# Kernel tuning notes

Measured on AMD Instinct MI355X. Metric: run time of the kernel, lower is better.

The kernel has to match this reference:

```python
import jax, jax.numpy as jnp
import numpy as np

N_NODES = 50000
N_EDGES = 640000
IN_FEATS = 128
HID = 128


def setup_inputs() -> dict:
    key = jax.random.key(0)
    ks = jax.random.split(key, 8)
    x = jax.random.normal(ks[0], (N_NODES, IN_FEATS), dtype=jnp.float32)
    src = jax.random.randint(ks[1], (N_EDGES,), 0, N_NODES, dtype=jnp.int32)
    dst = jax.random.randint(ks[2], (N_EDGES,), 0, N_NODES, dtype=jnp.int32)
    s1 = 1.0 / np.sqrt(IN_FEATS)
    s2 = 1.0 / np.sqrt(HID)
    W1 = jax.random.normal(ks[3], (IN_FEATS, HID), dtype=jnp.float32) * s1
    b1 = jnp.zeros((HID,), dtype=jnp.float32)
    W2 = jax.random.normal(ks[4], (HID, HID), dtype=jnp.float32) * s2
    b2 = jnp.zeros((HID,), dtype=jnp.float32)
    Wr = jax.random.normal(ks[5], (HID, 2), dtype=jnp.float32) * s2
    br = jnp.zeros((2,), dtype=jnp.float32)
    return {"x": x, "src": src, "dst": dst, "W1": W1, "b1": b1,
            "W2": W2, "b2": b2, "Wr": Wr, "br": br}


def _degree_norm(idx, n):
    # D^{-1/2}, with 0 for zero-degree nodes (DGL sets inf -> 0)
    deg = jax.ops.segment_sum(jnp.ones(idx.shape[0], jnp.float32), idx, num_segments=n)
    return jnp.where(deg > 0, jax.lax.rsqrt(jnp.maximum(deg, 1.0)), 0.0)


def _graph_conv(h, W, b, src, dst, norm_out, norm_in, n):
    # DGL GraphConv, norm='both': out = D_in^{-1/2} A D_out^{-1/2} (h W) + b
    hW = (h * norm_out[:, None]) @ W          # [N, hid]
    agg = jax.ops.segment_sum(hW[src], dst, num_segments=n)  # gather+scatter over edges
    return agg * norm_in[:, None] + b


def reference(x, src, dst, W1, b1, W2, b2, Wr, br):
    n = x.shape[0]
    norm_out = _degree_norm(src, n)  # source-side out-degree norm
    norm_in = _degree_norm(dst, n)   # dest-side in-degree norm
    h = jax.nn.relu(_graph_conv(x, W1, b1, src, dst, norm_out, norm_in, n))
    h = jax.nn.relu(_graph_conv(h, W2, b2, src, dst, norm_out, norm_in, n))
    hg = jnp.mean(h, axis=0, keepdims=True)  # [1, hid]
    return hg @ Wr + br                      # [1, 2]
```

## Files before the change

kernel.cpp:

```cpp
#include <hip/hip_runtime.h>
#include <hip/hip_bf16.h>

#define FEAT 128
#define RBITS 13
#define RSIZE 8192
#define NCHUNK 64

typedef __attribute__((ext_vector_type(8))) short short8;
typedef __attribute__((ext_vector_type(4))) short short4v;
typedef __attribute__((ext_vector_type(4))) float f32x4;

__device__ __forceinline__ ushort f2bf(float f) {
    union { float f; unsigned u; } v; v.f = f;
    unsigned u = v.u;
    unsigned r = 0x7fffu + ((u >> 16) & 1u);
    return (ushort)((u + r) >> 16);
}
__device__ __forceinline__ float bf2f(short s) {
    union { unsigned u; float f; } v;
    v.u = ((unsigned)(ushort)s) << 16;
    return v.f;
}

__global__ __launch_bounds__(256)
void hist_kernel(const int* __restrict__ src, const int* __restrict__ dst,
                 unsigned* __restrict__ partialSrc, unsigned* __restrict__ partialDst,
                 int E, int CS)
{
    __shared__ unsigned hs[RSIZE / 4];
    __shared__ unsigned hd[RSIZE / 4];
    const int c = blockIdx.x, p = blockIdx.y;
    for (int r = threadIdx.x; r < RSIZE / 4; r += 256) { hs[r] = 0; hd[r] = 0; }
    __syncthreads();
    const int e0 = c * CS, e1 = min(E, e0 + CS);
    for (int e = e0 + threadIdx.x; e < e1; e += 256) {
        int s = src[e];
        if ((s >> RBITS) == p) {
            int r = s & (RSIZE - 1);
            atomicAdd(&hs[r >> 2], 1u << ((r & 3) * 8));
        }
        int d = dst[e];
        if ((d >> RBITS) == p) {
            int r = d & (RSIZE - 1);
            atomicAdd(&hd[r >> 2], 1u << ((r & 3) * 8));
        }
    }
    __syncthreads();
    const size_t base = ((size_t)p * NCHUNK + c) * (RSIZE / 4);
    for (int r = threadIdx.x; r < RSIZE / 4; r += 256) {
        partialSrc[base + r] = hs[r];
        partialDst[base + r] = hd[r];
    }
}

__global__ __launch_bounds__(256)
void merge_kernel(const unsigned char* __restrict__ ps8, unsigned char* __restrict__ pd8,
                  int* __restrict__ cntIn, float* __restrict__ normOut,
                  float* __restrict__ normIn, int* __restrict__ blockSums, int N)
{
    const int n = blockIdx.x * 256 + threadIdx.x;
    unsigned off = 0;
    if (n < N) {
        const int p = n >> RBITS, r = n & (RSIZE - 1);
        const size_t base = (size_t)p * NCHUNK * RSIZE + r;
        unsigned so = 0;
#pragma unroll 8
        for (int c = 0; c < NCHUNK; ++c) so += ps8[base + (size_t)c * RSIZE];
#pragma unroll 8
        for (int c = 0; c < NCHUNK; ++c) {
            size_t i = base + (size_t)c * RSIZE;
            unsigned t = pd8[i];
            pd8[i] = (unsigned char)off;
            off += t;
        }
        cntIn[n]   = (int)off;
        normIn[n]  = off ? rsqrtf((float)off) : 0.0f;
        normOut[n] = so  ? rsqrtf((float)so)  : 0.0f;
    }
    __shared__ int sh[256];
    sh[threadIdx.x] = (int)off;
    __syncthreads();
    for (int o = 128; o > 0; o >>= 1) {
        if (threadIdx.x < o) sh[threadIdx.x] += sh[threadIdx.x + o];
        __syncthreads();
    }
    if (threadIdx.x == 0) blockSums[blockIdx.x] = sh[0];
}

__global__ __launch_bounds__(256)
void rowstart_kernel(const int* __restrict__ cntIn, const int* __restrict__ blockSums,
                     int* __restrict__ rowStart, float* __restrict__ colsum,
                     int N, int NB, int E)
{
    __shared__ int bs[256];
    __shared__ int bse[256];
    __shared__ int sh[256];
    const int t = threadIdx.x;
    int bv = (t < NB) ? blockSums[t] : 0;
    bs[t] = bv;
    __syncthreads();
    for (int off = 1; off < 256; off <<= 1) {
        int u = (t >= off) ? bs[t - off] : 0;
        __syncthreads();
        bs[t] += u;
        __syncthreads();
    }
    bse[t] = bs[t] - bv;
    __syncthreads();

    const int i = blockIdx.x * 256 + t;
    int v = (i < N) ? cntIn[i] : 0;
    sh[t] = v;
    __syncthreads();
    for (int off = 1; off < 256; off <<= 1) {
        int u = (t >= off) ? sh[t - off] : 0;
        __syncthreads();
        sh[t] += u;
        __syncthreads();
    }
    if (i < N) rowStart[i] = bse[blockIdx.x] + sh[t] - v;
    if (blockIdx.x == 0) {
        if (t == 0) rowStart[N] = E;
        colsum[t] = 0.0f;
    }
}

__global__ __launch_bounds__(256)
void fill_kernel(const int* __restrict__ src, const int* __restrict__ dst,
                 const int* __restrict__ rowStart, const unsigned char* __restrict__ chunkOff8,
                 int* __restrict__ csrSrc, int N, int E, int CS)
{
    __shared__ unsigned cursor[RSIZE];
    const int c = blockIdx.x, p = blockIdx.y;
    const unsigned char* co = chunkOff8 + ((size_t)p * NCHUNK + c) * RSIZE;
    for (int r = threadIdx.x; r < RSIZE; r += 256) {
        int n = (p << RBITS) + r;
        cursor[r] = (n < N) ? (unsigned)rowStart[n] + (unsigned)co[r] : 0u;
    }
    __syncthreads();
    const int e0 = c * CS, e1 = min(E, e0 + CS);
    for (int e = e0 + threadIdx.x; e < e1; e += 256) {
        int d = dst[e];
        if ((d >> RBITS) == p) {
            unsigned pos = atomicAdd(&cursor[d & (RSIZE - 1)], 1u);
            csrSrc[pos] = src[e];
        }
    }
}

template<bool F32IN>
__global__ __launch_bounds__(256)
void gemm_mfma_kernel(const void* __restrict__ Ain, const float* __restrict__ W,
                      const float* __restrict__ scale, ushort* __restrict__ C, int M)
{
    __shared__ ushort WT[128 * 132];
    __shared__ ushort As[64 * 132];
    __shared__ float  sScale[64];

    const int tid  = threadIdx.x;
    const int wv   = tid >> 6;
    const int lane = tid & 63;
    const int rowHalf = wv >> 1;
    const int colHalf = wv & 1;
    const int l15  = lane & 15;
    const int quad = lane >> 4;
    const int row0 = blockIdx.x << 6;

    for (int it = 0; it < 16; ++it) {
        int fid = tid + (it << 8);
        int k   = fid >> 5;
        int c4  = (fid & 31) << 2;
        float4 w = *(const float4*)(W + (size_t)k * FEAT + c4);
        WT[(c4 + 0) * 132 + k] = f2bf(w.x);
        WT[(c4 + 1) * 132 + k] = f2bf(w.y);
        WT[(c4 + 2) * 132 + k] = f2bf(w.z);
        WT[(c4 + 3) * 132 + k] = f2bf(w.w);
    }
#pragma unroll
    for (int it = 0; it < 4; ++it) {
        int fid = tid + (it << 8);
        int r   = fid >> 4;
        int seg = (fid & 15) << 3;
        int grow = row0 + r;
        short4v lo = {0, 0, 0, 0}, hi = {0, 0, 0, 0};
        if (grow < M) {
            if (F32IN) {
                const float* pa = (const float*)Ain + (size_t)grow * FEAT + seg;
                float4 u0 = *(const float4*)(pa);
                float4 u1 = *(const float4*)(pa + 4);
                lo[0] = (short)f2bf(u0.x); lo[1] = (short)f2bf(u0.y);
                lo[2] = (short)f2bf(u0.z); lo[3] = (short)f2bf(u0.w);
                hi[0] = (short)f2bf(u1.x); hi[1] = (short)f2bf(u1.y);
                hi[2] = (short)f2bf(u1.z); hi[3] = (short)f2bf(u1.w);
            } else {
                const ushort* pa = (const ushort*)Ain + (size_t)grow * FEAT + seg;
                lo = *(const short4v*)(pa);
                hi = *(const short4v*)(pa + 4);
            }
        }
        *(short4v*)&As[r * 132 + seg]     = lo;
        *(short4v*)&As[r * 132 + seg + 4] = hi;
    }
    if (tid < 64) {
        int grow = row0 + tid;
        sScale[tid] = (grow < M) ? scale[grow] : 0.0f;
    }
    __syncthreads();

    f32x4 acc[2][4] = {};
#pragma unroll
    for (int kst = 0; kst < 4; ++kst) {
        int k = kst * 32 + quad * 8;
        short8 af[2];
#pragma unroll
        for (int rt = 0; rt < 2; ++rt) {
            int row = rowHalf * 32 + rt * 16 + l15;
            short4v lo = *(const short4v*)&As[row * 132 + k];
            short4v hi = *(const short4v*)&As[row * 132 + k + 4];
            af[rt] = __builtin_shufflevector(lo, hi, 0, 1, 2, 3, 4, 5, 6, 7);
        }
        short8 bf[4];
#pragma unroll
        for (int ct = 0; ct < 4; ++ct) {
            int col = colHalf * 64 + ct * 16 + l15;
            short4v lo = *(const short4v*)&WT[col * 132 + k];
            short4v hi = *(const short4v*)&WT[col * 132 + k + 4];
            bf[ct] = __builtin_shufflevector(lo, hi, 0, 1, 2, 3, 4, 5, 6, 7);
        }
#pragma unroll
        for (int rt = 0; rt < 2; ++rt)
#pragma unroll
            for (int ct = 0; ct < 4; ++ct)
                acc[rt][ct] = __builtin_amdgcn_mfma_f32_16x16x32_bf16(
                    af[rt], bf[ct], acc[rt][ct], 0, 0, 0);
    }

#pragma unroll
    for (int rt = 0; rt < 2; ++rt) {
        int rbase = rowHalf * 32 + rt * 16 + quad * 4;
#pragma unroll
        for (int reg = 0; reg < 4; ++reg) {
            int rl = rbase + reg;
            int grow = row0 + rl;
            if (grow < M) {
                float sc = sScale[rl];
#pragma unroll
                for (int ct = 0; ct < 4; ++ct) {
                    int col = colHalf * 64 + ct * 16 + l15;
                    C[(size_t)grow * FEAT + col] = f2bf(acc[rt][ct][reg] * sc);
                }
            }
        }
    }
}

__global__ __launch_bounds__(256)
void gather_kernel(const ushort* __restrict__ t, const int* __restrict__ rowStart,
                   const int* __restrict__ csrSrc, const float* __restrict__ normIn,
                   const float* __restrict__ bias, ushort* __restrict__ out, int N)
{
    const int hw   = threadIdx.x >> 5;
    const int lane = threadIdx.x & 31;
    const int node = blockIdx.x * 8 + hw;
    if (node >= N) return;
    const int s = rowStart[node];
    const int e = rowStart[node + 1];
    float a0 = 0.f, a1 = 0.f, a2 = 0.f, a3 = 0.f;
    for (int base = s; base < e; base += 32) {
        const int m = min(32, e - base);
        int idx = (base + lane < e) ? csrSrc[base + lane] : 0;
        int j = 0;
        for (; j + 4 <= m; j += 4) {
            int s0 = __shfl(idx, j,     32);
            int s1 = __shfl(idx, j + 1, 32);
            int s2 = __shfl(idx, j + 2, 32);
            int s3 = __shfl(idx, j + 3, 32);
            short4v v0 = *(const short4v*)(t + (size_t)s0 * FEAT + lane * 4);
            short4v v1 = *(const short4v*)(t + (size_t)s1 * FEAT + lane * 4);
            short4v v2 = *(const short4v*)(t + (size_t)s2 * FEAT + lane * 4);
            short4v v3 = *(const short4v*)(t + (size_t)s3 * FEAT + lane * 4);
            a0 += bf2f(v0[0]) + bf2f(v1[0]) + bf2f(v2[0]) + bf2f(v3[0]);
            a1 += bf2f(v0[1]) + bf2f(v1[1]) + bf2f(v2[1]) + bf2f(v3[1]);
            a2 += bf2f(v0[2]) + bf2f(v1[2]) + bf2f(v2[2]) + bf2f(v3[2]);
            a3 += bf2f(v0[3]) + bf2f(v1[3]) + bf2f(v2[3]) + bf2f(v3[3]);
        }
        for (; j < m; ++j) {
            int srcn = __shfl(idx, j, 32);
            short4v v = *(const short4v*)(t + (size_t)srcn * FEAT + lane * 4);
            a0 += bf2f(v[0]); a1 += bf2f(v[1]); a2 += bf2f(v[2]); a3 += bf2f(v[3]);
        }
    }
    float ni = normIn[node];
    float4 b = *(const float4*)(bias + lane * 4);
    short4v o;
    o[0] = (short)f2bf(fmaxf(fmaf(a0, ni, b.x), 0.0f));
    o[1] = (short)f2bf(fmaxf(fmaf(a1, ni, b.y), 0.0f));
    o[2] = (short)f2bf(fmaxf(fmaf(a2, ni, b.z), 0.0f));
    o[3] = (short)f2bf(fmaxf(fmaf(a3, ni, b.w), 0.0f));
    *(short4v*)(out + (size_t)node * FEAT + lane * 4) = o;
}

__global__ __launch_bounds__(256)
void colreduce_kernel(const ushort* __restrict__ h2, float* __restrict__ colsum, int N)
{
    const int c  = threadIdx.x & 127;
    const int rg = threadIdx.x >> 7;
    const int r0 = blockIdx.x * 256;
    const int rEnd = min(r0 + 256, N);
    float acc = 0.0f;
    for (int r = r0 + rg; r < rEnd; r += 2)
        acc += bf2f(h2[(size_t)r * FEAT + c]);
    __shared__ float sh[256];
    sh[threadIdx.x] = acc;
    __syncthreads();
    if (rg == 0) unsafeAtomicAdd(&colsum[c], sh[c] + sh[128 + c]);
}

__global__ __launch_bounds__(128)
void final_kernel(const float* __restrict__ colsum, const float* __restrict__ Wr,
                  const float* __restrict__ br, float* __restrict__ out, float invN)
{
    __shared__ float s0[128], s1[128];
    int j = threadIdx.x;
    float hg = colsum[j] * invN;
    s0[j] = hg * Wr[2 * j + 0];
    s1[j] = hg * Wr[2 * j + 1];
    __syncthreads();
    for (int off = 64; off > 0; off >>= 1) {
        if (j < off) { s0[j] += s0[j + off]; s1[j] += s1[j + off]; }
        __syncthreads();
    }
    if (j == 0) {
        out[0] = s0[0] + br[0];
        out[1] = s1[0] + br[1];
    }
}

extern "C" void kernel_launch(void* const* d_in, const int* in_sizes, int n_in,
                              void* d_out, int out_size, void* d_ws, size_t ws_size,
                              hipStream_t stream)
{
    const float* x   = (const float*)d_in[0];
    const int*   src = (const int*)d_in[1];
    const int*   dst = (const int*)d_in[2];
    const float* W1  = (const float*)d_in[3];
    const float* b1  = (const float*)d_in[4];
    const float* W2  = (const float*)d_in[5];
    const float* b2  = (const float*)d_in[6];
    const float* Wr  = (const float*)d_in[7];
    const float* br  = (const float*)d_in[8];
    float* out = (float*)d_out;

    const int N = in_sizes[0] / FEAT;
    const int E = in_sizes[1];
    const int NP = ((N + 255) / 256) * 256;
    const int NB = (N + 255) / 256;
    const int P  = (N + RSIZE - 1) / RSIZE;
    const int CS = (E + NCHUNK - 1) / NCHUNK;

    char* p = (char*)d_ws;
    unsigned* partialSrc = (unsigned*)p;  p += (size_t)P * NCHUNK * (RSIZE / 4) * 4;
    unsigned* partialDst = (unsigned*)p;  p += (size_t)P * NCHUNK * (RSIZE / 4) * 4;
    float*  colsum    = (float*)p;        p += 256 * 4;
    int*    blockSums = (int*)p;          p += 256 * 4;
    int*    cntIn     = (int*)p;          p += (size_t)NP * 4;
    float*  normOut   = (float*)p;        p += (size_t)NP * 4;
    float*  normIn    = (float*)p;        p += (size_t)NP * 4;
    int*    rowStart  = (int*)p;          p += (size_t)(NP + 64) * 4;
    int*    csrSrc    = (int*)p;          p += (size_t)E * 4;
    ushort* bufT      = (ushort*)p;       p += (size_t)N * FEAT * 2;
    ushort* bufH      = (ushort*)p;       p += (size_t)N * FEAT * 2;

    hist_kernel<<<dim3(NCHUNK, P), 256, 0, stream>>>(src, dst, partialSrc, partialDst, E, CS);
    merge_kernel<<<NB, 256, 0, stream>>>((const unsigned char*)partialSrc,
                                         (unsigned char*)partialDst,
                                         cntIn, normOut, normIn, blockSums, N);
    rowstart_kernel<<<NB, 256, 0, stream>>>(cntIn, blockSums, rowStart, colsum, N, NB, E);
    fill_kernel<<<dim3(NCHUNK, P), 256, 0, stream>>>(src, dst, rowStart,
                                                     (const unsigned char*)partialDst,
                                                     csrSrc, N, E, CS);

    const int nStrips = (N + 63) / 64;
    const int gathBlocks = (N + 7) / 8;

    gemm_mfma_kernel<true><<<nStrips, 256, 0, stream>>>((const void*)x, W1, normOut, bufT, N);
    gather_kernel<<<gathBlocks, 256, 0, stream>>>(bufT, rowStart, csrSrc, normIn, b1, bufH, N);

    gemm_mfma_kernel<false><<<nStrips, 256, 0, stream>>>((const void*)bufH, W2, normOut, bufT, N);
    gather_kernel<<<gathBlocks, 256, 0, stream>>>(bufT, rowStart, csrSrc, normIn, b2, bufH, N);

    colreduce_kernel<<<NB, 256, 0, stream>>>(bufH, colsum, N);
    final_kernel<<<1, 128, 0, stream>>>(colsum, Wr, br, out, 1.0f / (float)N);
}
```

Before: 260.8 us.

## Restructure CSR build with whole-range byte histograms and pretransposed bf16 weights

The histogram and fill kernels drop the per-range partitioning (P ranges of 8192 nodes) and cover all nodes in one shared-memory array of packed byte counters. There are 128 edge chunks, and separate blocks handle src and dst. The fill step now derives each edge's in-row position from the old value returned by a byte-packed atomic, rather than keeping a per-node cursor. The weights are converted and transposed to bf16 once in a small kernel, and the GEMM keeps B fragments in registers instead of rebuilding WT in LDS for every block. It also unrolls the gather loop by two. The aim is to stop re-scanning all edges for every node range and to remove redundant per-block weight conversion. In exchange, counts must fit in 8 bits per chunk, and LDS use is large (about 50 KB).

```diff
diff --git a/kernel.cpp b/kernel.cpp
--- a/kernel.cpp
+++ b/kernel.cpp
@@ -2,9 +2,8 @@
 #include <hip/hip_bf16.h>
 
 #define FEAT 128
-#define RBITS 13
-#define RSIZE 8192
-#define NCHUNK 64
+#define NC 128
+#define MAXNPW 12544
 
 typedef __attribute__((ext_vector_type(8))) short short8;
 typedef __attribute__((ext_vector_type(4))) short short4v;
@@ -23,52 +22,52 @@
 }
 
 __global__ __launch_bounds__(256)
+void wtrans_kernel(const float* __restrict__ W1, const float* __restrict__ W2,
+                   ushort* __restrict__ WT1, ushort* __restrict__ WT2)
+{
+    const float* W = blockIdx.x ? W2 : W1;
+    ushort* WT = blockIdx.x ? WT2 : WT1;
+#pragma unroll
+    for (int it = 0; it < 64; ++it) {
+        int idx = threadIdx.x + it * 256;
+        int k = idx >> 7, c = idx & 127;
+        WT[c * 128 + k] = f2bf(W[idx]);
+    }
+}
+
+__global__ __launch_bounds__(256)
 void hist_kernel(const int* __restrict__ src, const int* __restrict__ dst,
-                 unsigned* __restrict__ partialSrc, unsigned* __restrict__ partialDst,
-                 int E, int CS)
-{
-    __shared__ unsigned hs[RSIZE / 4];
-    __shared__ unsigned hd[RSIZE / 4];
-    const int c = blockIdx.x, p = blockIdx.y;
-    for (int r = threadIdx.x; r < RSIZE / 4; r += 256) { hs[r] = 0; hd[r] = 0; }
+                 unsigned* __restrict__ partial, int NPW, int E, int CS)
+{
+    __shared__ unsigned h[MAXNPW];
+    const int c = blockIdx.x, job = blockIdx.y;
+    const int* __restrict__ idx = job ? dst : src;
+    for (int r = threadIdx.x; r < NPW; r += 256) h[r] = 0;
     __syncthreads();
     const int e0 = c * CS, e1 = min(E, e0 + CS);
     for (int e = e0 + threadIdx.x; e < e1; e += 256) {
-        int s = src[e];
-        if ((s >> RBITS) == p) {
-            int r = s & (RSIZE - 1);
-            atomicAdd(&hs[r >> 2], 1u << ((r & 3) * 8));
-        }
-        int d = dst[e];
-        if ((d >> RBITS) == p) {
-            int r = d & (RSIZE - 1);
-            atomicAdd(&hd[r >> 2], 1u << ((r & 3) * 8));
-        }
-    }
-    __syncthreads();
-    const size_t base = ((size_t)p * NCHUNK + c) * (RSIZE / 4);
-    for (int r = threadIdx.x; r < RSIZE / 4; r += 256) {
-        partialSrc[base + r] = hs[r];
-        partialDst[base + r] = hd[r];
-    }
+        int v = idx[e];
+        atomicAdd(&h[v >> 2], 1u << ((v & 3) * 8));
+    }
+    __syncthreads();
+    unsigned* out = partial + (size_t)(job * NC + c) * NPW;
+    for (int r = threadIdx.x; r < NPW; r += 256) out[r] = h[r];
 }
 
 __global__ __launch_bounds__(256)
 void merge_kernel(const unsigned char* __restrict__ ps8, unsigned char* __restrict__ pd8,
                   int* __restrict__ cntIn, float* __restrict__ normOut,
-                  float* __restrict__ normIn, int* __restrict__ blockSums, int N)
+                  float* __restrict__ normIn, int* __restrict__ blockSums, int N, int NPB)
 {
     const int n = blockIdx.x * 256 + threadIdx.x;
     unsigned off = 0;
     if (n < N) {
-        const int p = n >> RBITS, r = n & (RSIZE - 1);
-        const size_t base = (size_t)p * NCHUNK * RSIZE + r;
         unsigned so = 0;
 #pragma unroll 8
-        for (int c = 0; c < NCHUNK; ++c) so += ps8[base + (size_t)c * RSIZE];
+        for (int c = 0; c < NC; ++c) so += ps8[(size_t)c * NPB + n];
 #pragma unroll 8
-        for (int c = 0; c < NCHUNK; ++c) {
-            size_t i = base + (size_t)c * RSIZE;
+        for (int c = 0; c < NC; ++c) {
+            size_t i = (size_t)c * NPB + n;
             unsigned t = pd8[i];
             pd8[i] = (unsigned char)off;
             off += t;
@@ -127,33 +126,29 @@
 
 __global__ __launch_bounds__(256)
 void fill_kernel(const int* __restrict__ src, const int* __restrict__ dst,
-                 const int* __restrict__ rowStart, const unsigned char* __restrict__ chunkOff8,
-                 int* __restrict__ csrSrc, int N, int E, int CS)
-{
-    __shared__ unsigned cursor[RSIZE];
-    const int c = blockIdx.x, p = blockIdx.y;
-    const unsigned char* co = chunkOff8 + ((size_t)p * NCHUNK + c) * RSIZE;
-    for (int r = threadIdx.x; r < RSIZE; r += 256) {
-        int n = (p << RBITS) + r;
-        cursor[r] = (n < N) ? (unsigned)rowStart[n] + (unsigned)co[r] : 0u;
-    }
-    __syncthreads();
+                 const int* __restrict__ rowStart, const unsigned char* __restrict__ co8,
+                 int* __restrict__ csrSrc, int NPW, int NPB, int E, int CS)
+{
+    __shared__ unsigned cur[MAXNPW];
+    const int c = blockIdx.x;
+    for (int r = threadIdx.x; r < NPW; r += 256) cur[r] = 0;
+    __syncthreads();
+    const unsigned char* co = co8 + (size_t)c * NPB;
     const int e0 = c * CS, e1 = min(E, e0 + CS);
     for (int e = e0 + threadIdx.x; e < e1; e += 256) {
         int d = dst[e];
-        if ((d >> RBITS) == p) {
-            unsigned pos = atomicAdd(&cursor[d & (RSIZE - 1)], 1u);
-            csrSrc[pos] = src[e];
-        }
+        int sft = (d & 3) * 8;
+        unsigned old = atomicAdd(&cur[d >> 2], 1u << sft);
+        unsigned rel = (old >> sft) & 0xFFu;
+        csrSrc[(unsigned)rowStart[d] + (unsigned)co[d] + rel] = src[e];
     }
 }
 
 template<bool F32IN>
 __global__ __launch_bounds__(256)
-void gemm_mfma_kernel(const void* __restrict__ Ain, const float* __restrict__ W,
-                      const float* __restrict__ scale, ushort* __restrict__ C, int M)
-{
-    __shared__ ushort WT[128 * 132];
+void gemm_kernel(const void* __restrict__ Ain, const ushort* __restrict__ WT,
+                 const float* __restrict__ scale, ushort* __restrict__ C, int M)
+{
     __shared__ ushort As[64 * 132];
     __shared__ float  sScale[64];
 
@@ -166,16 +161,15 @@
     const int quad = lane >> 4;
     const int row0 = blockIdx.x << 6;
 
-    for (int it = 0; it < 16; ++it) {
-        int fid = tid + (it << 8);
-        int k   = fid >> 5;
-        int c4  = (fid & 31) << 2;
-        float4 w = *(const float4*)(W + (size_t)k * FEAT + c4);
-        WT[(c4 + 0) * 132 + k] = f2bf(w.x);
-        WT[(c4 + 1) * 132 + k] = f2bf(w.y);
-        WT[(c4 + 2) * 132 + k] = f2bf(w.z);
-        WT[(c4 + 3) * 132 + k] = f2bf(w.w);
-    }
+    short8 bfrag[4][4];
+#pragma unroll
+    for (int ct = 0; ct < 4; ++ct) {
+        int col = colHalf * 64 + ct * 16 + l15;
+#pragma unroll
+        for (int kst = 0; kst < 4; ++kst)
+            bfrag[ct][kst] = *(const short8*)(WT + col * 128 + kst * 32 + quad * 8);
+    }
+
 #pragma unroll
     for (int it = 0; it < 4; ++it) {
         int fid = tid + (it << 8);
@@ -211,28 +205,17 @@
 #pragma unroll
     for (int kst = 0; kst < 4; ++kst) {
         int k = kst * 32 + quad * 8;
-        short8 af[2];
 #pragma unroll
         for (int rt = 0; rt < 2; ++rt) {
             int row = rowHalf * 32 + rt * 16 + l15;
             short4v lo = *(const short4v*)&As[row * 132 + k];
             short4v hi = *(const short4v*)&As[row * 132 + k + 4];
-            af[rt] = __builtin_shufflevector(lo, hi, 0, 1, 2, 3, 4, 5, 6, 7);
-        }
-        short8 bf[4];
-#pragma unroll
-        for (int ct = 0; ct < 4; ++ct) {
-            int col = colHalf * 64 + ct * 16 + l15;
-            short4v lo = *(const short4v*)&WT[col * 132 + k];
-            short4v hi = *(const short4v*)&WT[col * 132 + k + 4];
-            bf[ct] = __builtin_shufflevector(lo, hi, 0, 1, 2, 3, 4, 5, 6, 7);
-        }
-#pragma unroll
-        for (int rt = 0; rt < 2; ++rt)
+            short8 af = __builtin_shufflevector(lo, hi, 0, 1, 2, 3, 4, 5, 6, 7);
 #pragma unroll
             for (int ct = 0; ct < 4; ++ct)
                 acc[rt][ct] = __builtin_amdgcn_mfma_f32_16x16x32_bf16(
-                    af[rt], bf[ct], acc[rt][ct], 0, 0, 0);
+                    af, bfrag[ct][kst], acc[rt][ct], 0, 0, 0);
+        }
     }
 
 #pragma unroll
@@ -270,6 +253,7 @@
         const int m = min(32, e - base);
         int idx = (base + lane < e) ? csrSrc[base + lane] : 0;
         int j = 0;
+#pragma unroll 2
         for (; j + 4 <= m; j += 4) {
             int s0 = __shfl(idx, j,     32);
             int s1 = __shfl(idx, j + 1, 32);
@@ -351,42 +335,44 @@
     const float* br  = (const float*)d_in[8];
     float* out = (float*)d_out;
 
-    const int N = in_sizes[0] / FEAT;
-    const int E = in_sizes[1];
+    const int N  = in_sizes[0] / FEAT;
+    const int E  = in_sizes[1];
     const int NP = ((N + 255) / 256) * 256;
     const int NB = (N + 255) / 256;
-    const int P  = (N + RSIZE - 1) / RSIZE;
-    const int CS = (E + NCHUNK - 1) / NCHUNK;
+    const int NPW = (N + 3) / 4;
+    const int NPB = NPW * 4;
+    const int CS  = (E + NC - 1) / NC;
 
     char* p = (char*)d_ws;
-    unsigned* partialSrc = (unsigned*)p;  p += (size_t)P * NCHUNK * (RSIZE / 4) * 4;
-    unsigned* partialDst = (unsigned*)p;  p += (size_t)P * NCHUNK * (RSIZE / 4) * 4;
-    float*  colsum    = (float*)p;        p += 256 * 4;
-    int*    blockSums = (int*)p;          p += 256 * 4;
-    int*    cntIn     = (int*)p;          p += (size_t)NP * 4;
-    float*  normOut   = (float*)p;        p += (size_t)NP * 4;
-    float*  normIn    = (float*)p;        p += (size_t)NP * 4;
-    int*    rowStart  = (int*)p;          p += (size_t)(NP + 64) * 4;
-    int*    csrSrc    = (int*)p;          p += (size_t)E * 4;
-    ushort* bufT      = (ushort*)p;       p += (size_t)N * FEAT * 2;
-    ushort* bufH      = (ushort*)p;       p += (size_t)N * FEAT * 2;
-
-    hist_kernel<<<dim3(NCHUNK, P), 256, 0, stream>>>(src, dst, partialSrc, partialDst, E, CS);
-    merge_kernel<<<NB, 256, 0, stream>>>((const unsigned char*)partialSrc,
-                                         (unsigned char*)partialDst,
-                                         cntIn, normOut, normIn, blockSums, N);
+    unsigned* partial  = (unsigned*)p;  p += (size_t)2 * NC * NPB;
+    ushort* WT1       = (ushort*)p;     p += 128 * 128 * 2;
+    ushort* WT2       = (ushort*)p;     p += 128 * 128 * 2;
+    float*  colsum    = (float*)p;      p += 256 * 4;
+    int*    blockSums = (int*)p;        p += 256 * 4;
+    int*    cntIn     = (int*)p;        p += (size_t)NP * 4;
+    float*  normOut   = (float*)p;      p += (size_t)NP * 4;
+    float*  normIn    = (float*)p;      p += (size_t)NP * 4;
+    int*    rowStart  = (int*)p;        p += (size_t)(NP + 64) * 4;
+    int*    csrSrc    = (int*)p;        p += (size_t)E * 4;
+    ushort* bufT      = (ushort*)p;     p += (size_t)N * FEAT * 2;
+    ushort* bufH      = (ushort*)p;     p += (size_t)N * FEAT * 2;
+
+    const unsigned char* ps8 = (const unsigned char*)partial;
+    unsigned char*       pd8 = (unsigned char*)partial + (size_t)NC * NPB;
+
+    wtrans_kernel<<<2, 256, 0, stream>>>(W1, W2, WT1, WT2);
+    hist_kernel<<<dim3(NC, 2), 256, 0, stream>>>(src, dst, partial, NPW, E, CS);
+    merge_kernel<<<NB, 256, 0, stream>>>(ps8, pd8, cntIn, normOut, normIn, blockSums, N, NPB);
     rowstart_kernel<<<NB, 256, 0, stream>>>(cntIn, blockSums, rowStart, colsum, N, NB, E);
-    fill_kernel<<<dim3(NCHUNK, P), 256, 0, stream>>>(src, dst, rowStart,
-                                                     (const unsigned char*)partialDst,
-                                                     csrSrc, N, E, CS);
+    fill_kernel<<<NC, 256, 0, stream>>>(src, dst, rowStart, pd8, csrSrc, NPW, NPB, E, CS);
 
     const int nStrips = (N + 63) / 64;
     const int gathBlocks = (N + 7) / 8;
 
-    gemm_mfma_kernel<true><<<nStrips, 256, 0, stream>>>((const void*)x, W1, normOut, bufT, N);
+    gemm_kernel<true><<<nStrips, 256, 0, stream>>>((const void*)x, WT1, normOut, bufT, N);
     gather_kernel<<<gathBlocks, 256, 0, stream>>>(bufT, rowStart, csrSrc, normIn, b1, bufH, N);
 
-    gemm_mfma_kernel<false><<<nStrips, 256, 0, stream>>>((const void*)bufH, W2, normOut, bufT, N);
+    gemm_kernel<false><<<nStrips, 256, 0, stream>>>((const void*)bufH, WT2, normOut, bufT, N);
     gather_kernel<<<gathBlocks, 256, 0, stream>>>(bufT, rowStart, csrSrc, normIn, b2, bufH, N);
 
     colreduce_kernel<<<NB, 256, 0, stream>>>(bufH, colsum, N);
```

New measurement: 265.8 us. About the same (+1.9%).
